# Optimization experiments

Measured on AMD Instinct MI355X. Metric: run time of the kernel, lower is better.

Reference implementation:

```python
import jax, jax.numpy as jnp
import numpy as np

MIN_HAIRPIN = 4
BIG = 1e30  # stand-in for the numpy reference's 1e18 INF (fp32-safe)


def _dp_single(e_pair, e_unp, allowed):
    """Nussinov min-energy DP for one sequence.
    e_pair: (L,L) f32, e_unp: (L,) f32, allowed: (L,L) bool.
    Returns dp (L,L) and ptr (L,L) backpointers matching the numpy reference:
      0 -> i unpaired, 1 -> j unpaired, 2 -> (i,j) paired, k+3 -> bifurcation at k.
    Vectorised over the antidiagonal (all i for a fixed span s at once).
    """
    L = e_unp.shape[0]
    idx = jnp.arange(L)
    dp0 = jnp.full((L, L), BIG, dtype=e_pair.dtype).at[idx, idx].set(e_unp)
    ptr0 = jnp.full((L, L), -1, dtype=jnp.int32).at[idx, idx].set(0)
    t = jnp.arange(L - 1)  # bifurcation offset k = i + t

    def step(carry, s):
        dp, ptr = carry
        j = idx + s - 1
        valid = j < L
        jc = jnp.minimum(j, L - 1)
        ip1 = jnp.minimum(idx + 1, L - 1)
        jm1 = jnp.maximum(jc - 1, 0)
        opt0 = dp[ip1, jc] + e_unp            # i unpaired
        opt1 = dp[idx, jm1] + e_unp[jc]       # j unpaired
        inner = jnp.where(s >= 3, dp[ip1, jm1], 0.0)
        pair_ok = allowed[idx, jc] & (s - 1 > MIN_HAIRPIN)  # j - i = s - 1
        opt2 = jnp.where(pair_ok, inner + e_pair[idx, jc], BIG)
        k = jnp.minimum(idx[:, None] + t[None, :], L - 1)
        bif = dp[idx[:, None], k] + dp[jnp.minimum(k + 1, L - 1), jc[:, None]]
        bif = jnp.where(t[None, :] < s - 1, bif, BIG)
        cand = jnp.concatenate([opt0[:, None], opt1[:, None], opt2[:, None], bif], axis=1)
        c = jnp.argmin(cand, axis=1)  # first-occurrence argmin == strict-< tie-break
        best = jnp.take_along_axis(cand, c[:, None], axis=1)[:, 0]
        new_ptr = jnp.where(c < 3, c, c + idx).astype(jnp.int32)  # c-3 is offset t -> k+3 = c+i
        dp = dp.at[idx, jc].set(jnp.where(valid, best, dp[idx, jc]))
        ptr = ptr.at[idx, jc].set(jnp.where(valid, new_ptr, ptr[idx, jc]))
        return (dp, ptr), None

    (dp, ptr), _ = jax.lax.scan(step, (dp0, ptr0), jnp.arange(2, L + 1))
    return dp, ptr


def _traceback(ptr):
    """Stack-based traceback of the backpointer matrix. Returns pairs (L,) int32, -1 = unpaired."""
    L = ptr.shape[0]

    def cond(st):
        return st[2] > 0

    def body(st):
        si, sj, sp, res = st
        top = sp - 1
        i, j = si[top], sj[top]
        skip = i >= j
        p = ptr[i, j]
        is0, is1, is2, isk = p == 0, p == 1, p == 2, p >= 3
        k = p - 3
        p1i = jnp.where(is0 | is2, i + 1, i)
        p1j = jnp.where(is1 | is2, j - 1, jnp.where(isk, k, j))
        v1 = (~skip) & jnp.where(is2, i + 1 <= j - 1, True)
        v2 = (~skip) & isk  # bifurcation pushes a second interval (k+1, j)
        res = jnp.where(is2 & (~skip), res.at[i].set(j).at[j].set(i), res)
        si = si.at[top].set(jnp.where(v1, p1i, si[top]))
        sj = sj.at[top].set(jnp.where(v1, p1j, sj[top]))
        slot2 = top + v1.astype(jnp.int32)
        si = si.at[slot2].set(jnp.where(v2, k + 1, si[slot2]))
        sj = sj.at[slot2].set(jnp.where(v2, j, sj[slot2]))
        sp = top + v1.astype(jnp.int32) + v2.astype(jnp.int32)
        return si, sj, sp, res

    si0 = jnp.zeros((L,), jnp.int32)
    sj0 = jnp.zeros((L,), jnp.int32).at[0].set(L - 1)
    res0 = jnp.full((L,), -1, jnp.int32)
    _, _, _, res = jax.lax.while_loop(cond, body, (si0, sj0, jnp.int32(1), res0))
    return res


def _structure_energy(e_pair, e_unp, pairs):
    """E(x,S) = sum_{i unpaired} e_unp[i] + sum_{(i,j) in S, i<j} e_pair[i,j]."""
    L = e_unp.shape[-1]
    clamped = jnp.maximum(pairs, 0)
    unp = jnp.where(pairs < 0, e_unp, 0.0).sum(-1)
    pe = jnp.take_along_axis(e_pair, clamped[..., None], axis=2)[..., 0]
    is_pair = (pairs >= 0) & (jnp.arange(L)[None, :] < clamped)
    return unp + jnp.where(is_pair, pe, 0.0).sum(-1)


def setup_inputs() -> dict:
    key = jax.random.key(0)
    k1, k2, k3 = jax.random.split(key, 3)
    B, L = 32, 384
    e_pair = jax.random.normal(k1, (B, L, L), jnp.float32)
    e_unp = jax.random.normal(k2, (B, L), jnp.float32)
    pair_mask = jax.random.randint(k3, (B, L, L), 0, 2).astype(jnp.bool_)
    return {"e_pair": e_pair, "e_unp": e_unp, "pair_mask": pair_mask}


def reference(e_pair, e_unp, pair_mask):
    dp, ptr = jax.vmap(_dp_single)(e_pair, e_unp, pair_mask)
    pairs = jax.vmap(_traceback)(ptr)  # (B, L) int32, -1 = unpaired
    energy = _structure_energy(e_pair, e_unp, pairs)  # (B,), equals dp[:, 0, -1]
    return pairs, energy
```

## Files before the change

### kernel.cpp

```cpp
#include <hip/hip_runtime.h>

#define LSEQ 384
#define BATCH 32
#define BIGV 1e30f
#define TB_STK 448
#define NN ((size_t)LSEQ * LSEQ)
#define BT 32
#define NT 12
#define PIT 33

__device__ __forceinline__ int detect_mmode_wave(const unsigned char* m0, int lane) {
    unsigned char v = m0[lane & 63];
    unsigned long long big = __ballot(v >= 2);
    unsigned long long off = __ballot((((lane & 63) & 3) != 0) && (v != 0));
    return big ? 2 : (off ? 1 : 0);
}
__device__ __forceinline__ bool mask_read(const void* mask, size_t idx, int mmode) {
    if (mmode == 0) return ((const unsigned int*)mask)[idx] != 0;
    if (mmode == 1) return ((const unsigned char*)mask)[idx] != 0;
    return ((const unsigned short*)mask)[idx] != 0;
}
__device__ __forceinline__ void choice_write(void* mask, size_t idx, int c, int mmode) {
    if (mmode == 0) ((unsigned int*)mask)[idx] = (unsigned int)c;
    else if (mmode == 1) ((unsigned char*)mask)[idx] = (unsigned char)c;
    else ((unsigned short*)mask)[idx] = (unsigned short)c;
}

__device__ __forceinline__ float edge_min32(const float* rowp, const float* colp) {
    float a0 = BIGV, a1 = BIGV, a2 = BIGV, a3 = BIGV;
    #pragma unroll
    for (int kk = 0; kk < 32; kk += 4) {
        float r0 = rowp[kk], r1 = rowp[kk + 1], r2 = rowp[kk + 2], r3 = rowp[kk + 3];
        const float* cb = colp + kk * PIT;
        float c0 = cb[0], c1 = cb[PIT], c2 = cb[2 * PIT], c3 = cb[3 * PIT];
        a0 = fminf(a0, r0 + c0); a1 = fminf(a1, r1 + c1);
        a2 = fminf(a2, r2 + c2); a3 = fminf(a3, r3 + c3);
    }
    return fminf(fminf(a0, a1), fminf(a2, a3));
}

__device__ __forceinline__ void minplus_waves(
    const float* __restrict__ dpG, int I, int J, const int* fm, int nfm,
    int wv, int lane, float part[4][BT][PIT])
{
    const int r0 = (lane >> 3) << 2, c0 = (lane & 7) << 2;
    float r16[16];
    #pragma unroll
    for (int z = 0; z < 16; ++z) r16[z] = BIGV;
    const int mi = wv >> 1, kqB = (wv & 1) * 4;
    if (mi < nfm) {
        const int M = fm[mi];
        #pragma unroll
        for (int q = 0; q < 4; ++q) {
            const int k = M * BT + (kqB + q) * 4;
            float4 a0 = *(const float4*)&dpG[(size_t)(I * BT + r0 + 0) * LSEQ + k];
            float4 a1 = *(const float4*)&dpG[(size_t)(I * BT + r0 + 1) * LSEQ + k];
            float4 a2 = *(const float4*)&dpG[(size_t)(I * BT + r0 + 2) * LSEQ + k];
            float4 a3 = *(const float4*)&dpG[(size_t)(I * BT + r0 + 3) * LSEQ + k];
            float4 b0 = *(const float4*)&dpG[(size_t)(J * BT + c0 + 0) * LSEQ + k];
            float4 b1 = *(const float4*)&dpG[(size_t)(J * BT + c0 + 1) * LSEQ + k];
            float4 b2 = *(const float4*)&dpG[(size_t)(J * BT + c0 + 2) * LSEQ + k];
            float4 b3 = *(const float4*)&dpG[(size_t)(J * BT + c0 + 3) * LSEQ + k];
            #pragma unroll
            for (int ri = 0; ri < 4; ++ri) {
                float4 av = ri == 0 ? a0 : ri == 1 ? a1 : ri == 2 ? a2 : a3;
                #pragma unroll
                for (int ci = 0; ci < 4; ++ci) {
                    float4 bv = ci == 0 ? b0 : ci == 1 ? b1 : ci == 2 ? b2 : b3;
                    float m = fminf(fminf(av.x + bv.x, av.y + bv.y),
                                    fminf(av.z + bv.z, av.w + bv.w));
                    r16[ri * 4 + ci] = fminf(r16[ri * 4 + ci], m);
                }
            }
        }
    }
    #pragma unroll
    for (int ri = 0; ri < 4; ++ri)
        #pragma unroll
        for (int ci = 0; ci < 4; ++ci)
            part[wv][r0 + ri][c0 + ci] = r16[ri * 4 + ci];
}

__device__ __constant__ int c_sb4[12] = {0,0,0,0, 0, 8, 15, 21, 26, 30, 33, 35};

__global__ __launch_bounds__(64) void diag_kernel(
    float* __restrict__ e_pair, const float* __restrict__ e_unp, void* mask)
{
    __shared__ float dT[BT + 1][PIT];
    __shared__ float epm[BT][PIT];
    __shared__ float s_eunp[BT];

    const int bid = blockIdx.x;
    const int b = bid / NT, t = bid % NT;
    const int lane = threadIdx.x;
    float* dpG = e_pair + (size_t)b * NN;
    const size_t mb = (size_t)b * NN;
    const int mmode = detect_mmode_wave((const unsigned char*)mask, lane);

    for (int z = lane; z < (BT + 1) * PIT; z += 64) ((float*)dT)[z] = BIGV;
    __syncthreads();
    if (lane < BT) {
        int i = t * BT + lane;
        float v = e_unp[b * LSEQ + i];
        s_eunp[lane] = v;
        dT[lane][lane] = v;
        dpG[(size_t)i * LSEQ + i] = v;
        if (i > 0) dpG[(size_t)i * LSEQ + i - 1] = v;
    }
    for (int z = lane; z < BT * BT; z += 64) {
        int li = z >> 5, lj = z & 31;
        int i = t * BT + li, j = t * BT + lj;
        bool ok = (lj - li > 4) && mask_read(mask, mb + (size_t)i * LSEQ + j, mmode);
        epm[li][lj] = ok ? dpG[(size_t)i * LSEQ + j] : BIGV;
    }
    __syncthreads();

    const int idx = lane >> 1, h = lane & 1;
    for (int sg = 1; sg < BT; ++sg) {
        const int nc = BT - sg;
        const bool act = idx < nc;
        const int li = idx, lj = idx + sg;
        const int ljc = lj < BT ? lj : BT - 1;
        const int i = t * BT + li, j = t * BT + lj;
        float ev = edge_min32(&dT[li][0], &dT[1][ljc]);
        float e1 = BIGV, opt0 = 0.f, x1 = BIGV, x2 = BIGV;
        if (act) {
            if (h == 0) {
                e1 = ev;
                opt0 = dT[li + 1][lj] + s_eunp[li];
            } else {
                x1 = dT[li][lj - 1] + s_eunp[lj];
                float pe = epm[li][lj];
                if (pe < BIGV) x2 = dT[li + 1][lj - 1] + pe;
            }
        }
        float y1 = __shfl_xor(x1, 1), y2 = __shfl_xor(x2, 1);
        if (act && h == 0) {
            float best = fminf(e1, y2);
            int cch = (best == opt0) ? 0 : (best == y1) ? 1
                     : (best == y2 && y2 < BIGV) ? 2 : 3;
            dT[li][lj] = best;
            dpG[(size_t)i * LSEQ + j] = best;
            if (i > 0) dpG[(size_t)j * LSEQ + i - 1] = best;
            choice_write(mask, mb + (size_t)j * LSEQ + i, cch, mmode);
        }
    }
}

__global__ __launch_bounds__(256) void step_kernel(
    float* __restrict__ e_pair, const float* __restrict__ e_unp,
    void* mask, float* __restrict__ acc, int p)
{
    __shared__ float dTI[BT + 1][PIT], dTJ[BT + 1][PIT];
    __shared__ float cur[BT + 1][PIT];
    __shared__ float epm[BT][PIT];
    __shared__ float part[4][BT][PIT];
    __shared__ float brow[BT], bcol[BT], s_eI[BT], s_eJ[BT];
    __shared__ float bcorn;

    const int b = blockIdx.x % BATCH;
    const int u = blockIdx.x / BATCH;
    const int nswp = NT - p;
    const int tid = threadIdx.x, lane = tid & 63, wv = tid >> 6;
    float* dpG = e_pair + (size_t)b * NN;
    const size_t mb = (size_t)b * NN;

    if (u >= nswp) {
        int e = u - nswp, s2 = p + 1;
        while (s2 < NT && e >= NT - s2) { e -= NT - s2; ++s2; }
        const int I = e, J = I + s2;
        int fm[2]; fm[0] = I + p - 1; int nfm = 1;
        if (J - (p - 1) != fm[0]) fm[nfm++] = J - (p - 1);
        minplus_waves(dpG, I, J, fm, nfm, wv, lane, part);
        __syncthreads();
        float* accT = acc + ((size_t)(b * 36 + c_sb4[s2] + I) << 10);
        const bool first = (p == (s2 + 1) / 2 + 1);
        for (int z = tid; z < BT * BT; z += 256) {
            int li = z >> 5, lj = z & 31;
            float m = fminf(fminf(part[0][li][lj], part[1][li][lj]),
                            fminf(part[2][li][lj], part[3][li][lj]));
            accT[z] = first ? m : fminf(accT[z], m);
        }
        return;
    }

    const int I = u, J = I + p, s = p;
    const int mmode = detect_mmode_wave((const unsigned char*)mask, lane);

    for (int z = tid; z < BT * BT; z += 256) {
        int li = z >> 5, lj = z & 31;
        dTI[li][lj] = (lj >= li) ? dpG[(size_t)(I * BT + li) * LSEQ + I * BT + lj] : BIGV;
        dTJ[li][lj] = (lj >= li) ? dpG[(size_t)(J * BT + li) * LSEQ + J * BT + lj] : BIGV;
    }
    for (int z = tid; z < PIT; z += 256) {
        dTI[BT][z] = BIGV; dTJ[BT][z] = BIGV; cur[BT][z] = BIGV;
    }
    if (tid < BT) {
        brow[tid] = dpG[(size_t)((I + 1) * BT) * LSEQ + J * BT + tid];
        s_eI[tid] = e_unp[b * LSEQ + I * BT + tid];
    } else if (tid < 2 * BT) {
        int q = tid - BT;
        bcol[q] = dpG[(size_t)(I * BT + q) * LSEQ + J * BT - 1];
        s_eJ[q] = e_unp[b * LSEQ + J * BT + q];
    } else if (tid == 2 * BT) {
        bcorn = (s >= 2) ? dpG[(size_t)((I + 1) * BT) * LSEQ + J * BT - 1] : BIGV;
    }
    for (int z = tid; z < BT * BT; z += 256) {
        int li = z >> 5, lj = z & 31;
        int i = I * BT + li, j = J * BT + lj;
        bool ok = (j - i > 4) && mask_read(mask, mb + (size_t)i * LSEQ + j, mmode);
        epm[li][lj] = ok ? dpG[(size_t)i * LSEQ + j] : BIGV;
    }

    int fm[2]; int nfm = 0;
    if (s >= 2) fm[nfm++] = I + 1;
    if (s >= 3) fm[nfm++] = J - 1;
    minplus_waves(dpG, I, J, fm, nfm, wv, lane, part);
    __syncthreads();

    const float* accT = acc + ((size_t)(b * 36 + c_sb4[s] + I) << 10);
    for (int z = tid; z < BT * BT; z += 256) {
        int li = z >> 5, lj = z & 31;
        float m = fminf(fminf(part[0][li][lj], part[1][li][lj]),
                        fminf(part[2][li][lj], part[3][li][lj]));
        if (s >= 4) m = fminf(m, accT[z]);
        cur[li][lj] = m;
    }
    __syncthreads();
    if (wv != 0) return;

    const int idx = lane >> 1, h = lane & 1;
    for (int sg = -(BT - 1); sg <= BT - 1; ++sg) {
        const int asg = sg < 0 ? -sg : sg;
        const int nc = BT - asg;
        const bool act = idx < nc;
        const int li = (sg >= 0) ? idx : idx - sg;
        const int lj = li + sg;
        const int lic = li < BT ? li : BT - 1;
        const int ljc = (lj < BT ? (lj >= 0 ? lj : 0) : BT - 1);
        const int i = I * BT + li, j = J * BT + lj;
        const float* rowp = (h == 0) ? &dTI[lic][0] : &cur[lic][0];
        const float* colp = (h == 0) ? &cur[1][ljc] : &dTJ[1][ljc];
        float ev = edge_min32(rowp, colp);
        float e1 = BIGV, opt0 = 0.f, farv = BIGV;
        float x0 = BIGV, x1 = BIGV, x2 = BIGV;
        if (act) {
            if (h == 0) {
                e1 = fminf(ev, dTI[li][BT - 1] + brow[lj]);
                opt0 = ((li + 1 < BT) ? cur[li + 1][lj] : brow[lj]) + s_eI[li];
                farv = cur[li][lj];
            } else {
                x0 = ev;
                x1 = ((lj >= 1) ? cur[li][lj - 1] : bcol[li]) + s_eJ[lj];
                float pe = epm[li][lj];
                if (pe < BIGV) {
                    float inner = (li + 1 < BT)
                        ? ((lj >= 1) ? cur[li + 1][lj - 1] : bcol[li + 1])
                        : ((lj >= 1) ? brow[lj - 1] : bcorn);
                    x2 = inner + pe;
                }
            }
        }
        float y0 = __shfl_xor(x0, 1), y1 = __shfl_xor(x1, 1), y2 = __shfl_xor(x2, 1);
        if (act && h == 0) {
            float best = fminf(fminf(fminf(e1, y0), farv), y2);
            int cch = (best == opt0) ? 0 : (best == y1) ? 1
                     : (best == y2 && y2 < BIGV) ? 2 : 3;
            cur[li][lj] = best;
            dpG[(size_t)i * LSEQ + j] = best;
            if (i > 0) dpG[(size_t)j * LSEQ + i - 1] = best;
            choice_write(mask, mb + (size_t)j * LSEQ + i, cch, mmode);
        }
    }
}

__global__ __launch_bounds__(512) void tb_kernel(
    const float* __restrict__ e_pair, const void* mask, float* __restrict__ out)
{
    const int b = blockIdx.x;
    const int tid = threadIdx.x;
    const int lane = tid & 63, wv = tid >> 6;
    const float* dp = e_pair + (size_t)b * NN;
    const size_t mb = (size_t)b * NN;
    const int mmode = detect_mmode_wave((const unsigned char*)mask, lane);

    __shared__ __align__(16) unsigned char ch[LSEQ * LSEQ];
    __shared__ short res[LSEQ];
    __shared__ int st[TB_STK];

    if (mmode == 1) {
        const uint4* src = (const uint4*)((const unsigned char*)mask + mb);
        for (int z = tid; z < (int)(NN / 16); z += 512) ((uint4*)ch)[z] = src[z];
    } else if (mmode == 2) {
        const uint4* src = (const uint4*)((const unsigned char*)mask + mb * 2);
        for (int z = tid; z < (int)(NN / 8); z += 512) {
            uint4 v = src[z];
            unsigned int lo = (v.x & 0xFFu) | (((v.x >> 16) & 0xFFu) << 8)
                            | ((v.y & 0xFFu) << 16) | (((v.y >> 16) & 0xFFu) << 24);
            unsigned int hi = (v.z & 0xFFu) | (((v.z >> 16) & 0xFFu) << 8)
                            | ((v.w & 0xFFu) << 16) | (((v.w >> 16) & 0xFFu) << 24);
            ((unsigned int*)ch)[z * 2] = lo;
            ((unsigned int*)ch)[z * 2 + 1] = hi;
        }
    } else {
        const uint4* src = (const uint4*)((const unsigned char*)mask + mb * 4);
        for (int z = tid; z < (int)(NN / 4); z += 512) {
            uint4 v = src[z];
            ((unsigned int*)ch)[z] = (v.x & 0xFFu) | ((v.y & 0xFFu) << 8)
                                   | ((v.z & 0xFFu) << 16) | ((v.w & 0xFFu) << 24);
        }
    }
    for (int l = tid; l < LSEQ; l += 512) res[l] = -1;
    __syncthreads();
    if (wv != 0) return;

    int sp = 0;
    int ci = 0, cj = LSEQ - 1;
    int have = 1;
    for (int iter = 0; iter < 8192; ++iter) {
        if (!have) {
            if (sp == 0) break;
            --sp;
            int pk = st[sp];
            ci = pk >> 16; cj = pk & 0xFFFF;
        }
        have = 0;
        if (ci >= cj) continue;
        int c = ch[(size_t)cj * LSEQ + ci];
        if (c == 0) { ++ci; have = 1; }
        else if (c == 1) { --cj; have = 1; }
        else if (c == 2) {
            res[ci] = (short)cj; res[cj] = (short)ci;
            if (ci + 1 <= cj - 1) { ++ci; --cj; have = 1; }
        } else {
            const int d = cj - ci;
            const float* rowi = dp + (size_t)ci * LSEQ;
            const float* mrow = dp + (size_t)cj * LSEQ;
            float bv = BIGV; int bt = d;
            for (int t = lane; t < d; t += 64) {
                float cc = rowi[ci + t] + mrow[ci + t];
                if (cc < bv || (cc == bv && t < bt)) { bv = cc; bt = t; }
            }
            for (int m = 32; m > 0; m >>= 1) {
                float ov = __shfl_xor(bv, m, 64);
                int   ot = __shfl_xor(bt, m, 64);
                if (ov < bv || (ov == bv && ot < bt)) { bv = ov; bt = ot; }
            }
            int k = ci + bt;
            if (sp < TB_STK - 1) { st[sp] = ((k + 1) << 16) | cj; ++sp; }
            cj = k; have = 1;
        }
    }

    for (int l = lane; l < LSEQ; l += 64)
        out[b * LSEQ + l] = (float)res[l];
    if (lane == 0)
        out[BATCH * LSEQ + b] = dp[LSEQ - 1];
}

extern "C" void kernel_launch(void* const* d_in, const int* in_sizes, int n_in,
                              void* d_out, int out_size, void* d_ws, size_t ws_size,
                              hipStream_t stream) {
    float* e_pair = (float*)d_in[0];
    const float* e_unp = (const float*)d_in[1];
    void* mask = d_in[2];
    float* acc = (float*)d_ws;
    (void)ws_size;

    static const int updC[12] = {0, 0, 0, 8, 13, 15, 14, 10, 6, 3, 1, 0};

    diag_kernel<<<BATCH * NT, 64, 0, stream>>>(e_pair, e_unp, mask);
    for (int p = 1; p < NT; ++p)
        step_kernel<<<BATCH * (NT - p + updC[p]), 256, 0, stream>>>(
            e_pair, e_unp, mask, acc, p);
    tb_kernel<<<BATCH, 512, 0, stream>>>(e_pair, mask, (float*)d_out);
}
```

Before: 775.6 us.

## Fuse diagonal tiles and first off-diagonal sweep; copy only lower-triangle choices in traceback

Replaces the diagonal-tile kernel and the p=1 step kernel with a single kernel in which each block computes two adjacent diagonal tiles (in two waves) and then sweeps the tile between them. This removes one launch and a global-memory round trip between the two stages, at the cost of recomputing each interior diagonal tile in two blocks (only one of them writes it). The traceback kernel now copies only the lower-triangle part of each row of the choice matrix into shared memory, which roughly halves the bytes it loads. The step kernel also now loads the pair energy before the mask check.

After: 776.7 us. About the same (+0.1%).

```diff
diff --git a/kernel.cpp b/kernel.cpp
--- a/kernel.cpp
+++ b/kernel.cpp
@@ -8,6 +8,8 @@
 #define BT 32
 #define NT 12
 #define PIT 33
+
+__device__ __constant__ int c_sb4[12] = {0,0,0,0, 0, 8, 15, 21, 26, 30, 33, 35};
 
 __device__ __forceinline__ int detect_mmode_wave(const unsigned char* m0, int lane) {
     unsigned char v = m0[lane & 63];
@@ -81,40 +83,10 @@
             part[wv][r0 + ri][c0 + ci] = r16[ri * 4 + ci];
 }
 
-__device__ __constant__ int c_sb4[12] = {0,0,0,0, 0, 8, 15, 21, 26, 30, 33, 35};
-
-__global__ __launch_bounds__(64) void diag_kernel(
-    float* __restrict__ e_pair, const float* __restrict__ e_unp, void* mask)
-{
-    __shared__ float dT[BT + 1][PIT];
-    __shared__ float epm[BT][PIT];
-    __shared__ float s_eunp[BT];
-
-    const int bid = blockIdx.x;
-    const int b = bid / NT, t = bid % NT;
-    const int lane = threadIdx.x;
-    float* dpG = e_pair + (size_t)b * NN;
-    const size_t mb = (size_t)b * NN;
-    const int mmode = detect_mmode_wave((const unsigned char*)mask, lane);
-
-    for (int z = lane; z < (BT + 1) * PIT; z += 64) ((float*)dT)[z] = BIGV;
-    __syncthreads();
-    if (lane < BT) {
-        int i = t * BT + lane;
-        float v = e_unp[b * LSEQ + i];
-        s_eunp[lane] = v;
-        dT[lane][lane] = v;
-        dpG[(size_t)i * LSEQ + i] = v;
-        if (i > 0) dpG[(size_t)i * LSEQ + i - 1] = v;
-    }
-    for (int z = lane; z < BT * BT; z += 64) {
-        int li = z >> 5, lj = z & 31;
-        int i = t * BT + li, j = t * BT + lj;
-        bool ok = (lj - li > 4) && mask_read(mask, mb + (size_t)i * LSEQ + j, mmode);
-        epm[li][lj] = ok ? dpG[(size_t)i * LSEQ + j] : BIGV;
-    }
-    __syncthreads();
-
+__device__ void diag_sweep(float (*dT)[PIT], const float (*epm)[PIT],
+                           const float* eunp, int t, float* __restrict__ dpG,
+                           size_t mb, void* mask, int mmode, int lane, int dowrite)
+{
     const int idx = lane >> 1, h = lane & 1;
     for (int sg = 1; sg < BT; ++sg) {
         const int nc = BT - sg;
@@ -127,9 +99,9 @@
         if (act) {
             if (h == 0) {
                 e1 = ev;
-                opt0 = dT[li + 1][lj] + s_eunp[li];
+                opt0 = dT[li + 1][lj] + eunp[li];
             } else {
-                x1 = dT[li][lj - 1] + s_eunp[lj];
+                x1 = dT[li][lj - 1] + eunp[lj];
                 float pe = epm[li][lj];
                 if (pe < BIGV) x2 = dT[li + 1][lj - 1] + pe;
             }
@@ -140,95 +112,22 @@
             int cch = (best == opt0) ? 0 : (best == y1) ? 1
                      : (best == y2 && y2 < BIGV) ? 2 : 3;
             dT[li][lj] = best;
-            dpG[(size_t)i * LSEQ + j] = best;
-            if (i > 0) dpG[(size_t)j * LSEQ + i - 1] = best;
-            choice_write(mask, mb + (size_t)j * LSEQ + i, cch, mmode);
-        }
-    }
-}
-
-__global__ __launch_bounds__(256) void step_kernel(
-    float* __restrict__ e_pair, const float* __restrict__ e_unp,
-    void* mask, float* __restrict__ acc, int p)
-{
-    __shared__ float dTI[BT + 1][PIT], dTJ[BT + 1][PIT];
-    __shared__ float cur[BT + 1][PIT];
-    __shared__ float epm[BT][PIT];
-    __shared__ float part[4][BT][PIT];
-    __shared__ float brow[BT], bcol[BT], s_eI[BT], s_eJ[BT];
-    __shared__ float bcorn;
-
-    const int b = blockIdx.x % BATCH;
-    const int u = blockIdx.x / BATCH;
-    const int nswp = NT - p;
-    const int tid = threadIdx.x, lane = tid & 63, wv = tid >> 6;
-    float* dpG = e_pair + (size_t)b * NN;
-    const size_t mb = (size_t)b * NN;
-
-    if (u >= nswp) {
-        int e = u - nswp, s2 = p + 1;
-        while (s2 < NT && e >= NT - s2) { e -= NT - s2; ++s2; }
-        const int I = e, J = I + s2;
-        int fm[2]; fm[0] = I + p - 1; int nfm = 1;
-        if (J - (p - 1) != fm[0]) fm[nfm++] = J - (p - 1);
-        minplus_waves(dpG, I, J, fm, nfm, wv, lane, part);
-        __syncthreads();
-        float* accT = acc + ((size_t)(b * 36 + c_sb4[s2] + I) << 10);
-        const bool first = (p == (s2 + 1) / 2 + 1);
-        for (int z = tid; z < BT * BT; z += 256) {
-            int li = z >> 5, lj = z & 31;
-            float m = fminf(fminf(part[0][li][lj], part[1][li][lj]),
-                            fminf(part[2][li][lj], part[3][li][lj]));
-            accT[z] = first ? m : fminf(accT[z], m);
-        }
-        return;
-    }
-
-    const int I = u, J = I + p, s = p;
-    const int mmode = detect_mmode_wave((const unsigned char*)mask, lane);
-
-    for (int z = tid; z < BT * BT; z += 256) {
-        int li = z >> 5, lj = z & 31;
-        dTI[li][lj] = (lj >= li) ? dpG[(size_t)(I * BT + li) * LSEQ + I * BT + lj] : BIGV;
-        dTJ[li][lj] = (lj >= li) ? dpG[(size_t)(J * BT + li) * LSEQ + J * BT + lj] : BIGV;
-    }
-    for (int z = tid; z < PIT; z += 256) {
-        dTI[BT][z] = BIGV; dTJ[BT][z] = BIGV; cur[BT][z] = BIGV;
-    }
-    if (tid < BT) {
-        brow[tid] = dpG[(size_t)((I + 1) * BT) * LSEQ + J * BT + tid];
-        s_eI[tid] = e_unp[b * LSEQ + I * BT + tid];
-    } else if (tid < 2 * BT) {
-        int q = tid - BT;
-        bcol[q] = dpG[(size_t)(I * BT + q) * LSEQ + J * BT - 1];
-        s_eJ[q] = e_unp[b * LSEQ + J * BT + q];
-    } else if (tid == 2 * BT) {
-        bcorn = (s >= 2) ? dpG[(size_t)((I + 1) * BT) * LSEQ + J * BT - 1] : BIGV;
-    }
-    for (int z = tid; z < BT * BT; z += 256) {
-        int li = z >> 5, lj = z & 31;
-        int i = I * BT + li, j = J * BT + lj;
-        bool ok = (j - i > 4) && mask_read(mask, mb + (size_t)i * LSEQ + j, mmode);
-        epm[li][lj] = ok ? dpG[(size_t)i * LSEQ + j] : BIGV;
-    }
-
-    int fm[2]; int nfm = 0;
-    if (s >= 2) fm[nfm++] = I + 1;
-    if (s >= 3) fm[nfm++] = J - 1;
-    minplus_waves(dpG, I, J, fm, nfm, wv, lane, part);
-    __syncthreads();
-
-    const float* accT = acc + ((size_t)(b * 36 + c_sb4[s] + I) << 10);
-    for (int z = tid; z < BT * BT; z += 256) {
-        int li = z >> 5, lj = z & 31;
-        float m = fminf(fminf(part[0][li][lj], part[1][li][lj]),
-                        fminf(part[2][li][lj], part[3][li][lj]));
-        if (s >= 4) m = fminf(m, accT[z]);
-        cur[li][lj] = m;
-    }
-    __syncthreads();
-    if (wv != 0) return;
-
+            if (dowrite) {
+                dpG[(size_t)i * LSEQ + j] = best;
+                if (i > 0) dpG[(size_t)j * LSEQ + i - 1] = best;
+                choice_write(mask, mb + (size_t)j * LSEQ + i, cch, mmode);
+            }
+        }
+    }
+}
+
+__device__ void sweep_wave(
+    const float (*dTI)[PIT], const float (*dTJ)[PIT], float (*cur)[PIT],
+    const float (*epm)[PIT], const float* eI, const float* eJ,
+    const float* brow, const float* bcol, float bcorn,
+    int I, int J, float* __restrict__ dpG, size_t mb, void* mask, int mmode,
+    int lane)
+{
     const int idx = lane >> 1, h = lane & 1;
     for (int sg = -(BT - 1); sg <= BT - 1; ++sg) {
         const int asg = sg < 0 ? -sg : sg;
@@ -247,11 +146,11 @@
         if (act) {
             if (h == 0) {
                 e1 = fminf(ev, dTI[li][BT - 1] + brow[lj]);
-                opt0 = ((li + 1 < BT) ? cur[li + 1][lj] : brow[lj]) + s_eI[li];
+                opt0 = ((li + 1 < BT) ? cur[li + 1][lj] : brow[lj]) + eI[li];
                 farv = cur[li][lj];
             } else {
                 x0 = ev;
-                x1 = ((lj >= 1) ? cur[li][lj - 1] : bcol[li]) + s_eJ[lj];
+                x1 = ((lj >= 1) ? cur[li][lj - 1] : bcol[li]) + eJ[lj];
                 float pe = epm[li][lj];
                 if (pe < BIGV) {
                     float inner = (li + 1 < BT)
@@ -274,6 +173,165 @@
     }
 }
 
+__global__ __launch_bounds__(256) void fused_d1_kernel(
+    float* __restrict__ e_pair, const float* __restrict__ e_unp, void* mask)
+{
+    __shared__ float dA[BT + 1][PIT], dB[BT + 1][PIT], cur[BT + 1][PIT];
+    __shared__ float epmA[BT][PIT], epmB[BT][PIT], epmS[BT][PIT];
+    __shared__ float eA[BT], eB[BT], brow[BT], bcol[BT];
+
+    const int b = blockIdx.x % BATCH;
+    const int I = blockIdx.x / BATCH;
+    const int tid = threadIdx.x, lane = tid & 63, wv = tid >> 6;
+    float* dpG = e_pair + (size_t)b * NN;
+    const size_t mb = (size_t)b * NN;
+    const int mmode = detect_mmode_wave((const unsigned char*)mask, lane);
+
+    for (int z = tid; z < (BT + 1) * PIT; z += 256) {
+        ((float*)dA)[z] = BIGV; ((float*)dB)[z] = BIGV; ((float*)cur)[z] = BIGV;
+    }
+    if (tid < BT) eA[tid] = e_unp[b * LSEQ + I * BT + tid];
+    else if (tid < 2 * BT) eB[tid - BT] = e_unp[b * LSEQ + (I + 1) * BT + (tid - BT)];
+    __syncthreads();
+
+    if (tid < BT) {
+        int i = I * BT + tid;
+        float v = eA[tid];
+        dA[tid][tid] = v;
+        if (I == 0) {
+            dpG[(size_t)i * LSEQ + i] = v;
+            if (i > 0) dpG[(size_t)i * LSEQ + i - 1] = v;
+        }
+    } else if (tid < 2 * BT) {
+        int q = tid - BT, i = (I + 1) * BT + q;
+        float v = eB[q];
+        dB[q][q] = v;
+        dpG[(size_t)i * LSEQ + i] = v;
+        dpG[(size_t)i * LSEQ + i - 1] = v;
+    }
+    for (int z = tid; z < BT * BT; z += 256) {
+        int li = z >> 5, lj = z & 31;
+        {
+            int i = I * BT + li, j = I * BT + lj;
+            float pv = dpG[(size_t)i * LSEQ + j];
+            bool ok = (lj - li > 4) && mask_read(mask, mb + (size_t)i * LSEQ + j, mmode);
+            epmA[li][lj] = ok ? pv : BIGV;
+        }
+        {
+            int i = (I + 1) * BT + li, j = (I + 1) * BT + lj;
+            float pv = dpG[(size_t)i * LSEQ + j];
+            bool ok = (lj - li > 4) && mask_read(mask, mb + (size_t)i * LSEQ + j, mmode);
+            epmB[li][lj] = ok ? pv : BIGV;
+        }
+        {
+            int i = I * BT + li, j = (I + 1) * BT + lj;
+            float pv = dpG[(size_t)i * LSEQ + j];
+            bool ok = (j - i > 4) && mask_read(mask, mb + (size_t)i * LSEQ + j, mmode);
+            epmS[li][lj] = ok ? pv : BIGV;
+        }
+    }
+    __syncthreads();
+
+    if (wv == 0)      diag_sweep(dA, epmA, eA, I, dpG, mb, mask, mmode, lane, I == 0);
+    else if (wv == 1) diag_sweep(dB, epmB, eB, I + 1, dpG, mb, mask, mmode, lane, 1);
+    __syncthreads();
+
+    if (tid < BT) brow[tid] = dB[0][tid];
+    else if (tid < 2 * BT) bcol[tid - BT] = dA[tid - BT][BT - 1];
+    __syncthreads();
+
+    if (wv == 0)
+        sweep_wave(dA, dB, cur, epmS, eA, eB, brow, bcol, BIGV,
+                   I, I + 1, dpG, mb, mask, mmode, lane);
+}
+
+__global__ __launch_bounds__(256) void step_kernel(
+    float* __restrict__ e_pair, const float* __restrict__ e_unp,
+    void* mask, float* __restrict__ acc, int p)
+{
+    __shared__ float dTI[BT + 1][PIT], dTJ[BT + 1][PIT];
+    __shared__ float cur[BT + 1][PIT];
+    __shared__ float epm[BT][PIT];
+    __shared__ float part[4][BT][PIT];
+    __shared__ float brow[BT], bcol[BT], s_eI[BT], s_eJ[BT];
+    __shared__ float bcorn;
+
+    const int b = blockIdx.x % BATCH;
+    const int u = blockIdx.x / BATCH;
+    const int nswp = NT - p;
+    const int tid = threadIdx.x, lane = tid & 63, wv = tid >> 6;
+    float* dpG = e_pair + (size_t)b * NN;
+    const size_t mb = (size_t)b * NN;
+
+    if (u >= nswp) {
+        int e = u - nswp, s2 = p + 1;
+        while (s2 < NT && e >= NT - s2) { e -= NT - s2; ++s2; }
+        const int I = e, J = I + s2;
+        int fm[2]; fm[0] = I + p - 1; int nfm = 1;
+        if (J - (p - 1) != fm[0]) fm[nfm++] = J - (p - 1);
+        minplus_waves(dpG, I, J, fm, nfm, wv, lane, part);
+        __syncthreads();
+        float* accT = acc + ((size_t)(b * 36 + c_sb4[s2] + I) << 10);
+        const bool first = (p == (s2 + 1) / 2 + 1);
+        for (int z = tid; z < BT * BT; z += 256) {
+            int li = z >> 5, lj = z & 31;
+            float m = fminf(fminf(part[0][li][lj], part[1][li][lj]),
+                            fminf(part[2][li][lj], part[3][li][lj]));
+            accT[z] = first ? m : fminf(accT[z], m);
+        }
+        return;
+    }
+
+    const int I = u, J = I + p, s = p;
+    const int mmode = detect_mmode_wave((const unsigned char*)mask, lane);
+
+    for (int z = tid; z < BT * BT; z += 256) {
+        int li = z >> 5, lj = z & 31;
+        dTI[li][lj] = (lj >= li) ? dpG[(size_t)(I * BT + li) * LSEQ + I * BT + lj] : BIGV;
+        dTJ[li][lj] = (lj >= li) ? dpG[(size_t)(J * BT + li) * LSEQ + J * BT + lj] : BIGV;
+    }
+    for (int z = tid; z < PIT; z += 256) {
+        dTI[BT][z] = BIGV; dTJ[BT][z] = BIGV; cur[BT][z] = BIGV;
+    }
+    if (tid < BT) {
+        brow[tid] = dpG[(size_t)((I + 1) * BT) * LSEQ + J * BT + tid];
+        s_eI[tid] = e_unp[b * LSEQ + I * BT + tid];
+    } else if (tid < 2 * BT) {
+        int q = tid - BT;
+        bcol[q] = dpG[(size_t)(I * BT + q) * LSEQ + J * BT - 1];
+        s_eJ[q] = e_unp[b * LSEQ + J * BT + q];
+    } else if (tid == 2 * BT) {
+        bcorn = (s >= 2) ? dpG[(size_t)((I + 1) * BT) * LSEQ + J * BT - 1] : BIGV;
+    }
+    for (int z = tid; z < BT * BT; z += 256) {
+        int li = z >> 5, lj = z & 31;
+        int i = I * BT + li, j = J * BT + lj;
+        float pv = dpG[(size_t)i * LSEQ + j];
+        bool ok = (j - i > 4) && mask_read(mask, mb + (size_t)i * LSEQ + j, mmode);
+        epm[li][lj] = ok ? pv : BIGV;
+    }
+
+    int fm[2]; int nfm = 0;
+    if (s >= 2) fm[nfm++] = I + 1;
+    if (s >= 3) fm[nfm++] = J - 1;
+    minplus_waves(dpG, I, J, fm, nfm, wv, lane, part);
+    __syncthreads();
+
+    const float* accT = acc + ((size_t)(b * 36 + c_sb4[s] + I) << 10);
+    for (int z = tid; z < BT * BT; z += 256) {
+        int li = z >> 5, lj = z & 31;
+        float m = fminf(fminf(part[0][li][lj], part[1][li][lj]),
+                        fminf(part[2][li][lj], part[3][li][lj]));
+        if (s >= 4) m = fminf(m, accT[z]);
+        cur[li][lj] = m;
+    }
+    __syncthreads();
+    if (wv != 0) return;
+
+    sweep_wave(dTI, dTJ, cur, epm, s_eI, s_eJ, brow, bcol, bcorn,
+               I, J, dpG, mb, mask, mmode, lane);
+}
+
 __global__ __launch_bounds__(512) void tb_kernel(
     const float* __restrict__ e_pair, const void* mask, float* __restrict__ out)
 {
@@ -289,25 +347,45 @@
     __shared__ int st[TB_STK];
 
     if (mmode == 1) {
-        const uint4* src = (const uint4*)((const unsigned char*)mask + mb);
-        for (int z = tid; z < (int)(NN / 16); z += 512) ((uint4*)ch)[z] = src[z];
+        for (int j = wv; j < LSEQ; j += 8) {
+            const uint4* src = (const uint4*)((const unsigned char*)mask + mb + (size_t)j * LSEQ);
+            uint4* dst = (uint4*)(ch + (size_t)j * LSEQ);
+            const int nch = (j + 15) >> 4;
+            for (int c = lane; c < nch; c += 64) dst[c] = src[c];
+        }
     } else if (mmode == 2) {
-        const uint4* src = (const uint4*)((const unsigned char*)mask + mb * 2);
-        for (int z = tid; z < (int)(NN / 8); z += 512) {
-            uint4 v = src[z];
-            unsigned int lo = (v.x & 0xFFu) | (((v.x >> 16) & 0xFFu) << 8)
-                            | ((v.y & 0xFFu) << 16) | (((v.y >> 16) & 0xFFu) << 24);
-            unsigned int hi = (v.z & 0xFFu) | (((v.z >> 16) & 0xFFu) << 8)
-                            | ((v.w & 0xFFu) << 16) | (((v.w >> 16) & 0xFFu) << 24);
-            ((unsigned int*)ch)[z * 2] = lo;
-            ((unsigned int*)ch)[z * 2 + 1] = hi;
+        for (int j = wv; j < LSEQ; j += 8) {
+            const uint4* src = (const uint4*)((const unsigned short*)mask + mb + (size_t)j * LSEQ);
+            uint4* dst = (uint4*)(ch + (size_t)j * LSEQ);
+            const int nch = (j + 15) >> 4;
+            for (int c = lane; c < nch; c += 64) {
+                uint4 v0 = src[2 * c], v1 = src[2 * c + 1];
+                uint4 o;
+                o.x = (v0.x & 0xFFu) | (((v0.x >> 16) & 0xFFu) << 8)
+                    | ((v0.y & 0xFFu) << 16) | (((v0.y >> 16) & 0xFFu) << 24);
+                o.y = (v0.z & 0xFFu) | (((v0.z >> 16) & 0xFFu) << 8)
+                    | ((v0.w & 0xFFu) << 16) | (((v0.w >> 16) & 0xFFu) << 24);
+                o.z = (v1.x & 0xFFu) | (((v1.x >> 16) & 0xFFu) << 8)
+                    | ((v1.y & 0xFFu) << 16) | (((v1.y >> 16) & 0xFFu) << 24);
+                o.w = (v1.z & 0xFFu) | (((v1.z >> 16) & 0xFFu) << 8)
+                    | ((v1.w & 0xFFu) << 16) | (((v1.w >> 16) & 0xFFu) << 24);
+                dst[c] = o;
+            }
         }
     } else {
-        const uint4* src = (const uint4*)((const unsigned char*)mask + mb * 4);
-        for (int z = tid; z < (int)(NN / 4); z += 512) {
-            uint4 v = src[z];
-            ((unsigned int*)ch)[z] = (v.x & 0xFFu) | ((v.y & 0xFFu) << 8)
-                                   | ((v.z & 0xFFu) << 16) | ((v.w & 0xFFu) << 24);
+        for (int j = wv; j < LSEQ; j += 8) {
+            const uint4* src = (const uint4*)((const unsigned int*)mask + mb + (size_t)j * LSEQ);
+            uint4* dst = (uint4*)(ch + (size_t)j * LSEQ);
+            const int nch = (j + 15) >> 4;
+            for (int c = lane; c < nch; c += 64) {
+                uint4 s0 = src[4 * c], s1 = src[4 * c + 1], s2 = src[4 * c + 2], s3 = src[4 * c + 3];
+                uint4 o;
+                o.x = (s0.x & 0xFFu) | ((s0.y & 0xFFu) << 8) | ((s0.z & 0xFFu) << 16) | ((s0.w & 0xFFu) << 24);
+                o.y = (s1.x & 0xFFu) | ((s1.y & 0xFFu) << 8) | ((s1.z & 0xFFu) << 16) | ((s1.w & 0xFFu) << 24);
+                o.z = (s2.x & 0xFFu) | ((s2.y & 0xFFu) << 8) | ((s2.z & 0xFFu) << 16) | ((s2.w & 0xFFu) << 24);
+                o.w = (s3.x & 0xFFu) | ((s3.y & 0xFFu) << 8) | ((s3.z & 0xFFu) << 16) | ((s3.w & 0xFFu) << 24);
+                dst[c] = o;
+            }
         }
     }
     for (int l = tid; l < LSEQ; l += 512) res[l] = -1;
@@ -369,8 +447,8 @@
 
     static const int updC[12] = {0, 0, 0, 8, 13, 15, 14, 10, 6, 3, 1, 0};
 
-    diag_kernel<<<BATCH * NT, 64, 0, stream>>>(e_pair, e_unp, mask);
-    for (int p = 1; p < NT; ++p)
+    fused_d1_kernel<<<BATCH * (NT - 1), 256, 0, stream>>>(e_pair, e_unp, mask);
+    for (int p = 2; p < NT; ++p)
         step_kernel<<<BATCH * (NT - p + updC[p]), 256, 0, stream>>>(
             e_pair, e_unp, mask, acc, p);
     tb_kernel<<<BATCH, 512, 0, stream>>>(e_pair, mask, (float*)d_out);
```
